# Performance work log

Measured on AMD Instinct MI355X. Metric: run time of the kernel, lower is better.

Reference implementation:

```python
import jax, jax.numpy as jnp
import numpy as np

T, B, IN, H = 512, 64, 1024, 1024


def setup_inputs() -> dict:
    key = jax.random.key(0)
    ks = jax.random.split(key, 10)
    s_in = 1.0 / np.sqrt(IN)
    s_h = 1.0 / np.sqrt(H)
    return {
        "input": jax.random.normal(ks[0], (T, B, IN), dtype=jnp.float32),
        "h_0": jax.random.normal(ks[1], (2, B, H), dtype=jnp.float32),
        "W_ih0": jax.random.uniform(ks[2], (H, IN), jnp.float32, -s_in, s_in),
        "b_ih0": jax.random.uniform(ks[3], (H,), jnp.float32, -s_in, s_in),
        "W_hh0": jax.random.uniform(ks[4], (H, H), jnp.float32, -s_h, s_h),
        "b_hh0": jax.random.uniform(ks[5], (H,), jnp.float32, -s_h, s_h),
        "W_ih1": jax.random.uniform(ks[6], (H, H), jnp.float32, -s_h, s_h),
        "b_ih1": jax.random.uniform(ks[7], (H,), jnp.float32, -s_h, s_h),
        "W_hh1": jax.random.uniform(ks[8], (H, H), jnp.float32, -s_h, s_h),
        "b_hh1": jax.random.uniform(ks[9], (H,), jnp.float32, -s_h, s_h),
    }


def reference(input, h_0, W_ih0, b_ih0, W_hh0, b_hh0, W_ih1, b_ih1, W_hh1, b_hh1):
    # input: [T, B, IN] (time-major); h_0: [2, B, H]
    def step(carry, x):
        h0, h1 = carry
        h0 = jnp.tanh(x @ W_ih0.T + b_ih0 + h0 @ W_hh0.T + b_hh0)
        h1 = jnp.tanh(h0 @ W_ih1.T + b_ih1 + h1 @ W_hh1.T + b_hh1)
        return (h0, h1), h1

    (h0_n, h1_n), outputs = jax.lax.scan(step, (h_0[0], h_0[1]), input)
    return outputs, jnp.stack([h0_n, h1_n])
```

## Files before the change

kernel.cpp:

```cpp
#include <hip/hip_runtime.h>
#include <math.h>

#define TT 512
#define BB 64
#define HH 1024
#define KK 2048
#define NWGL 128
#define ROWS 8
#define RING_D 8
#define BH (BB*HH)
#define WSTRIDE 76
#define NSH 8
#define SHTGT (NWGL/NSH)

#define LDS_FLOATS (16384 + 4*64*WSTRIDE + 2048)

typedef float floatx4 __attribute__((ext_vector_type(4)));


__device__ __forceinline__ void spin_ge(int* p, int target) {
    int it = 0;
    while (__hip_atomic_load(p, __ATOMIC_RELAXED, __HIP_MEMORY_SCOPE_AGENT) < target) {
        __builtin_amdgcn_s_sleep(16);
        if (++it > (1 << 16)) return;
    }
}

__device__ __forceinline__ void st_agent(float* p, float v) {
    __hip_atomic_store(p, v, __ATOMIC_RELAXED, __HIP_MEMORY_SCOPE_AGENT);
}

#define FMA8(s, iv) \
    acc[s][0] += wA.x*(iv); acc[s][1] += wA.y*(iv); acc[s][2] += wA.z*(iv); acc[s][3] += wA.w*(iv); \
    acc[s][4] += wB.x*(iv); acc[s][5] += wB.y*(iv); acc[s][6] += wB.z*(iv); acc[s][7] += wB.w*(iv);

#define STAGE_WRITE_COMPUTE(v, c) do {                                         \
    const int k0_ = kq + (c) * 64;                                             \
    _Pragma("unroll")                                                          \
    for (int i = 0; i < 16; ++i) {                                             \
        const int b = i * 4 + bsub;                                            \
        *(float4*)(bufW + b * WSTRIDE + kk4) =                                 \
            make_float4(v[i][0], v[i][1], v[i][2], v[i][3]);                   \
    }                                                                          \
    const float* wt = Wt + (size_t)(wof + k0_ + g) * 8;                        \
    const float* bw = bufW + b16 * WSTRIDE + g;                                \
    _Pragma("unroll 4")                                                        \
    for (int j = 0; j < 16; ++j) {                                             \
        const float4 wA = *(const float4*)(wt + j * 32);                       \
        const float4 wB = *(const float4*)(wt + j * 32 + 4);                   \
        const float i0 = bw[j * 4];                                            \
        const float i1 = bw[j * 4 + 16 * WSTRIDE];                             \
        const float i2 = bw[j * 4 + 32 * WSTRIDE];                             \
        const float i3 = bw[j * 4 + 48 * WSTRIDE];                             \
        FMA8(0, i0) FMA8(1, i1) FMA8(2, i2) FMA8(3, i3)                        \
    }                                                                          \
} while (0)

#define ISSUE16(v, c) do {                                                     \
    _Pragma("unroll")                                                          \
    for (int i = 0; i < 16; ++i) {                                             \
        const float* p = src + (i * 4 + bsub) * 1024 + kq + (c) * 64 + kk4;    \
        asm volatile("global_load_dwordx4 %0, %1, off sc1"                     \
                     : "=v"(v[i]) : "v"(p));                                   \
    }                                                                          \
} while (0)

template<bool BYPASS>
__device__ __forceinline__ void stage_and_accum(
    const float* __restrict__ src,
    const float* __restrict__ Wt,
    float* __restrict__ bufW,
    int kq,
    int wof,
    int lane,
    float acc[4][8])
{
    const int bsub = lane >> 4;
    const int kk4  = (lane & 15) * 4;
    const int b16  = lane & 15;
    const int g    = bsub;
    if (BYPASS) {
        floatx4 vA[16], vB[16];
        ISSUE16(vA, 0);
        ISSUE16(vB, 1);
        asm volatile("s_waitcnt vmcnt(16)" ::: "memory");
        __builtin_amdgcn_sched_barrier(0);
        STAGE_WRITE_COMPUTE(vA, 0);
        ISSUE16(vA, 2);
        asm volatile("s_waitcnt vmcnt(16)" ::: "memory");
        __builtin_amdgcn_sched_barrier(0);
        STAGE_WRITE_COMPUTE(vB, 1);
        ISSUE16(vB, 3);
        asm volatile("s_waitcnt vmcnt(16)" ::: "memory");
        __builtin_amdgcn_sched_barrier(0);
        STAGE_WRITE_COMPUTE(vA, 2);
        asm volatile("s_waitcnt vmcnt(0)" ::: "memory");
        __builtin_amdgcn_sched_barrier(0);
        STAGE_WRITE_COMPUTE(vB, 3);
    } else {
        #pragma unroll 1
        for (int c = 0; c < 4; ++c) {
            const int k0 = kq + c * 64;
            floatx4 vc[16];
            #pragma unroll
            for (int i = 0; i < 16; ++i) {
                const float4 t4 = *(const float4*)(src + (i * 4 + bsub) * 1024 + k0 + kk4);
                vc[i][0] = t4.x; vc[i][1] = t4.y; vc[i][2] = t4.z; vc[i][3] = t4.w;
            }
            STAGE_WRITE_COMPUTE(vc, c);
        }
    }
}

extern "C" __global__ void rnn_init(int* __restrict__ c) {
    const int i = blockIdx.x * blockDim.x + threadIdx.x;
    if (i < 2 * NSH * TT) c[i] = 0;
}

extern "C" __global__ void __launch_bounds__(256, 1)
rnn_persist(const float* __restrict__ x,
            const float* __restrict__ h0init,
            const float* __restrict__ Wih0, const float* __restrict__ bih0,
            const float* __restrict__ Whh0, const float* __restrict__ bhh0,
            const float* __restrict__ Wih1, const float* __restrict__ bih1,
            const float* __restrict__ Whh1, const float* __restrict__ bhh1,
            float* __restrict__ out,
            int* __restrict__ c0, int* __restrict__ c1,
            float* __restrict__ ring)
{
    extern __shared__ float lds[];
    float* Wt    = lds;
    float* buf   = lds + ROWS * KK;
    float* parts = buf + 4 * 64 * WSTRIDE;

    const int wg   = blockIdx.x;
    const bool isL1 = (wg >= NWGL);
    const int g    = isL1 ? wg - NWGL : wg;
    const int rbase = g * ROWS;
    const int sh   = g & (NSH - 1);
    const int tid  = threadIdx.x;
    const int wv   = tid >> 6;
    const int lane = tid & 63;
    const int kq   = wv * 256;
    float* bufW = buf + wv * (64 * WSTRIDE);

    const float* Wa = isL1 ? Wih1 : Wih0;
    const float* Wb = isL1 ? Whh1 : Whh0;
    for (int idx = tid; idx < ROWS * 1024; idx += 256) {
        const int r = idx >> 10;
        const int k = idx & 1023;
        Wt[(size_t)k * 8 + r]          = Wa[(size_t)(rbase + r) * HH + k];
        Wt[(size_t)(1024 + k) * 8 + r] = Wb[(size_t)(rbase + r) * HH + k];
    }
    const int er = tid & 7;
    const float bsum = isL1 ? (bih1[rbase + er] + bhh1[rbase + er])
                            : (bih0[rbase + er] + bhh0[rbase + er]);
    __syncthreads();

    const int gk = lane >> 4;

    for (int t = 0; t < TT; ++t) {
        float acc[4][8];
        #pragma unroll
        for (int s = 0; s < 4; ++s)
            #pragma unroll
            for (int r = 0; r < 8; ++r) acc[s][r] = 0.f;

        if (!isL1) {
            stage_and_accum<false>(x + (size_t)t * BH, Wt, bufW, kq, 0, lane, acc);
            if (wv == 0) {
                int* a = nullptr;
                if (lane < 8) { if (t >= 1) a = c0 + lane * TT + (t - 1); }
                else if (lane < 16 && t >= RING_D) a = c1 + (lane - 8) * TT + (t - RING_D);
                if (a) spin_ge(a, SHTGT);
            }
            __syncthreads();
            const float* hp = (t == 0) ? h0init
                                       : ring + (size_t)((t - 1) % RING_D) * BH;
            stage_and_accum<true>(hp, Wt, bufW, kq, 1024, lane, acc);
        } else {
            if (wv == 0 && lane < 8 && t >= 1)
                spin_ge(c1 + lane * TT + (t - 1), SHTGT);
            __syncthreads();
            const float* hp = (t == 0) ? (h0init + BH)
                                       : (out + (size_t)(t - 1) * BH);
            stage_and_accum<true>(hp, Wt, bufW, kq, 1024, lane, acc);
            if (wv == 0 && lane < 8)
                spin_ge(c0 + lane * TT + t, SHTGT);
            __syncthreads();
            stage_and_accum<true>(ring + (size_t)(t % RING_D) * BH, Wt, bufW, kq, 0, lane, acc);
        }

        float outv[8];
        #pragma unroll
        for (int r = 0; r < 8; ++r) {
            #pragma unroll
            for (int s = 0; s < 4; ++s) {
                float v = acc[s][r];
                v += __shfl_xor(v, 16, 64);
                v += __shfl_xor(v, 32, 64);
                acc[s][r] = v;
            }
            float v = acc[0][r];
            if (gk == 1) v = acc[1][r];
            if (gk == 2) v = acc[2][r];
            if (gk == 3) v = acc[3][r];
            outv[r] = v;
        }

        float* pw = parts + (size_t)(wv * 64 + lane) * ROWS;
        *(float4*)(pw + 0) = make_float4(outv[0], outv[1], outv[2], outv[3]);
        *(float4*)(pw + 4) = make_float4(outv[4], outv[5], outv[6], outv[7]);
        __syncthreads();

        for (int o = tid; o < 512; o += 256) {
            const int b = o >> 3;
            const int r = o & 7;
            const float s = parts[o] + parts[o + 512] + parts[o + 1024] + parts[o + 1536] + bsum;
            const float hv = tanhf(s);
            const int col = rbase + r;
            if (!isL1) {
                st_agent(ring + (size_t)(t % RING_D) * BH + b * HH + col, hv);
                if (t == TT - 1) st_agent(out + (size_t)TT * BH + b * HH + col, hv);
            } else {
                st_agent(out + (size_t)t * BH + b * HH + col, hv);
                if (t == TT - 1) st_agent(out + (size_t)TT * BH + BH + b * HH + col, hv);
            }
        }
        __syncthreads();
        if (tid == 0) {
            asm volatile("s_waitcnt vmcnt(0)" ::: "memory");
            __hip_atomic_fetch_add((isL1 ? c1 : c0) + sh * TT + t, 1,
                                   __ATOMIC_RELAXED, __HIP_MEMORY_SCOPE_AGENT);
        }
    }
}

extern "C" void kernel_launch(void* const* d_in, const int* in_sizes, int n_in,
                              void* d_out, int out_size, void* d_ws, size_t ws_size,
                              hipStream_t stream) {
    const float* x    = (const float*)d_in[0];
    const float* h0i  = (const float*)d_in[1];
    const float* Wih0 = (const float*)d_in[2];
    const float* bih0 = (const float*)d_in[3];
    const float* Whh0 = (const float*)d_in[4];
    const float* bhh0 = (const float*)d_in[5];
    const float* Wih1 = (const float*)d_in[6];
    const float* bih1 = (const float*)d_in[7];
    const float* Whh1 = (const float*)d_in[8];
    const float* bhh1 = (const float*)d_in[9];
    float* out = (float*)d_out;

    int*   c0   = (int*)d_ws;
    int*   c1   = c0 + NSH * TT;
    float* ring = (float*)((char*)d_ws + 65536);

    (void)hipFuncSetAttribute((const void*)rnn_persist,
                              hipFuncAttributeMaxDynamicSharedMemorySize,
                              LDS_FLOATS * 4);

    rnn_init<<<32, 256, 0, stream>>>(c0);
    rnn_persist<<<256, 256, LDS_FLOATS * 4, stream>>>(
        x, h0i, Wih0, bih0, Whh0, bhh0, Wih1, bih1, Whh1, bhh1,
        out, c0, c1, ring);
}
```

Before: 13.37 ms.

## Replace sharded atomic counters with per-workgroup step flags polled wave-wide

Each workgroup used to do an atomic fetch-add on one of 8 sharded per-timestep counters, and 8 or 16 lanes spun on those counters. Now each workgroup stores its completed step number into its own flag slot, padded to 4 ints. The 64 lanes of a wave poll all 128 flags, two per lane, and use __all to decide when to proceed, with a shorter sleep between polls. This removes atomic read-modify-write contention and shortens the wake-up latency of the barrier. In exchange, every poll issues more loads, which adds memory traffic while waiting.

Measured after the change: 12.54 ms. -6.2%, faster.

```diff
diff --git a/kernel.cpp b/kernel.cpp
--- a/kernel.cpp
+++ b/kernel.cpp
@@ -10,20 +10,15 @@
 #define RING_D 8
 #define BH (BB*HH)
 #define WSTRIDE 76
-#define NSH 8
-#define SHTGT (NWGL/NSH)
+#define FSTR 4
 
 #define LDS_FLOATS (16384 + 4*64*WSTRIDE + 2048)
 
 typedef float floatx4 __attribute__((ext_vector_type(4)));
 
 
-__device__ __forceinline__ void spin_ge(int* p, int target) {
-    int it = 0;
-    while (__hip_atomic_load(p, __ATOMIC_RELAXED, __HIP_MEMORY_SCOPE_AGENT) < target) {
-        __builtin_amdgcn_s_sleep(16);
-        if (++it > (1 << 16)) return;
-    }
+__device__ __forceinline__ int ld_flag(const int* p) {
+    return __hip_atomic_load(p, __ATOMIC_RELAXED, __HIP_MEMORY_SCOPE_AGENT);
 }
 
 __device__ __forceinline__ void st_agent(float* p, float v) {
@@ -114,7 +109,7 @@
 
 extern "C" __global__ void rnn_init(int* __restrict__ c) {
     const int i = blockIdx.x * blockDim.x + threadIdx.x;
-    if (i < 2 * NSH * TT) c[i] = 0;
+    if (i < 2 * NWGL * FSTR) c[i] = 0;
 }
 
 extern "C" __global__ void __launch_bounds__(256, 1)
@@ -125,7 +120,7 @@
             const float* __restrict__ Wih1, const float* __restrict__ bih1,
             const float* __restrict__ Whh1, const float* __restrict__ bhh1,
             float* __restrict__ out,
-            int* __restrict__ c0, int* __restrict__ c1,
+            int* __restrict__ f0, int* __restrict__ f1,
             float* __restrict__ ring)
 {
     extern __shared__ float lds[];
@@ -137,7 +132,6 @@
     const bool isL1 = (wg >= NWGL);
     const int g    = isL1 ? wg - NWGL : wg;
     const int rbase = g * ROWS;
-    const int sh   = g & (NSH - 1);
     const int tid  = threadIdx.x;
     const int wv   = tid >> 6;
     const int lane = tid & 63;
@@ -158,6 +152,10 @@
     __syncthreads();
 
     const int gk = lane >> 4;
+    const int* p0a = f0 + lane * FSTR;
+    const int* p0b = f0 + (lane + 64) * FSTR;
+    const int* p1a = f1 + lane * FSTR;
+    const int* p1b = f1 + (lane + 64) * FSTR;
 
     for (int t = 0; t < TT; ++t) {
         float acc[4][8];
@@ -168,25 +166,44 @@
 
         if (!isL1) {
             stage_and_accum<false>(x + (size_t)t * BH, Wt, bufW, kq, 0, lane, acc);
-            if (wv == 0) {
-                int* a = nullptr;
-                if (lane < 8) { if (t >= 1) a = c0 + lane * TT + (t - 1); }
-                else if (lane < 16 && t >= RING_D) a = c1 + (lane - 8) * TT + (t - RING_D);
-                if (a) spin_ge(a, SHTGT);
+            if (wv == 0 && t >= 1) {
+                const int tr = t - RING_D + 1;
+                int it = 0;
+                for (;;) {
+                    bool ok = (ld_flag(p0a) >= t) & (ld_flag(p0b) >= t);
+                    if (t >= RING_D)
+                        ok = ok & (ld_flag(p1a) >= tr) & (ld_flag(p1b) >= tr);
+                    if (__all(ok)) break;
+                    __builtin_amdgcn_s_sleep(2);
+                    if (++it > (1 << 15)) break;
+                }
             }
             __syncthreads();
             const float* hp = (t == 0) ? h0init
                                        : ring + (size_t)((t - 1) % RING_D) * BH;
             stage_and_accum<true>(hp, Wt, bufW, kq, 1024, lane, acc);
         } else {
-            if (wv == 0 && lane < 8 && t >= 1)
-                spin_ge(c1 + lane * TT + (t - 1), SHTGT);
+            if (wv == 0 && t >= 1) {
+                int it = 0;
+                for (;;) {
+                    if (__all((ld_flag(p1a) >= t) & (ld_flag(p1b) >= t))) break;
+                    __builtin_amdgcn_s_sleep(2);
+                    if (++it > (1 << 15)) break;
+                }
+            }
             __syncthreads();
             const float* hp = (t == 0) ? (h0init + BH)
                                        : (out + (size_t)(t - 1) * BH);
             stage_and_accum<true>(hp, Wt, bufW, kq, 1024, lane, acc);
-            if (wv == 0 && lane < 8)
-                spin_ge(c0 + lane * TT + t, SHTGT);
+            if (wv == 0) {
+                const int tp = t + 1;
+                int it = 0;
+                for (;;) {
+                    if (__all((ld_flag(p0a) >= tp) & (ld_flag(p0b) >= tp))) break;
+                    __builtin_amdgcn_s_sleep(2);
+                    if (++it > (1 << 15)) break;
+                }
+            }
             __syncthreads();
             stage_and_accum<true>(ring + (size_t)(t % RING_D) * BH, Wt, bufW, kq, 0, lane, acc);
         }
@@ -230,8 +247,8 @@
         __syncthreads();
         if (tid == 0) {
             asm volatile("s_waitcnt vmcnt(0)" ::: "memory");
-            __hip_atomic_fetch_add((isL1 ? c1 : c0) + sh * TT + t, 1,
-                                   __ATOMIC_RELAXED, __HIP_MEMORY_SCOPE_AGENT);
+            __hip_atomic_store((isL1 ? f1 : f0) + g * FSTR, t + 1,
+                               __ATOMIC_RELAXED, __HIP_MEMORY_SCOPE_AGENT);
         }
     }
 }
@@ -251,16 +268,16 @@
     const float* bhh1 = (const float*)d_in[9];
     float* out = (float*)d_out;
 
-    int*   c0   = (int*)d_ws;
-    int*   c1   = c0 + NSH * TT;
+    int*   f0   = (int*)d_ws;
+    int*   f1   = f0 + NWGL * FSTR;
     float* ring = (float*)((char*)d_ws + 65536);
 
     (void)hipFuncSetAttribute((const void*)rnn_persist,
                               hipFuncAttributeMaxDynamicSharedMemorySize,
                               LDS_FLOATS * 4);
 
-    rnn_init<<<32, 256, 0, stream>>>(c0);
+    rnn_init<<<4, 256, 0, stream>>>(f0);
     rnn_persist<<<256, 256, LDS_FLOATS * 4, stream>>>(
         x, h0i, Wih0, bih0, Whh0, bhh0, Wih1, bih1, Whh1, bhh1,
-        out, c0, c1, ring);
-}
+        out, f0, f1, ring);
+}
```
